# Kernel tuning notes

Hardware: AMD Instinct MI355X
Metric: run time of the kernel (lower is better)

The kernel has to match this reference:

```python
import jax, jax.numpy as jnp
import numpy as np

NUM_COLORS = 10
COLOR_MAPPING_W = 0.4
CONSISTENCY_W = 0.3
RULE_W = 0.2
EXACT_BONUS = 5.0


def _color_rules(targets, num_colors):
    # Vectorized equivalent of per-batch torch.unique(): sorted unique colors
    # of each grid written into the first slots of a [B, 10] rules tensor.
    B = targets.shape[0]
    colors = jnp.arange(num_colors)
    presence = jnp.any(targets[:, :, :, None] == colors, axis=(1, 2))  # [B, 10]
    pos = jnp.cumsum(presence.astype(jnp.int32), axis=1) - 1           # slot index per color
    cols = jnp.where(presence, pos, num_colors)                        # absent -> dump slot
    rules = jnp.zeros((B, num_colors + 1), dtype=jnp.float32)
    rules = rules.at[jnp.arange(B)[:, None], cols].set(
        colors.astype(jnp.float32) * presence.astype(jnp.float32))
    return rules[:, :num_colors]


def setup_inputs() -> dict:
    key = jax.random.key(0)
    k1, k2, k3, k4 = jax.random.split(key, 4)
    B, C, H, W = 4096, NUM_COLORS, 30, 30
    return {
        "color_output": jax.random.normal(k1, (B, C, H, W), dtype=jnp.float32),
        "targets": jax.random.randint(k2, (B, H, W), 0, C),
        "color_attention": jax.random.uniform(k3, (B, H, W, C), dtype=jnp.float32),
        "lstm_rules": jax.random.normal(k4, (B, C), dtype=jnp.float32),
    }


def reference(color_output, targets, color_attention, lstm_rules):
    B, C, H, W = color_output.shape
    # exact-match cross entropy (mean over B*H*W)
    logp = jax.nn.log_softmax(color_output, axis=1)               # [B,C,H,W]
    ce = -jnp.take_along_axis(logp, targets[:, None], axis=1).mean()
    pred_colors = jnp.argmax(color_output, axis=1)                # [B,H,W]
    eq = (pred_colors == targets).astype(jnp.float32)
    exact_count = eq.sum()
    # color mapping: MSE(attention, one_hot(targets))
    onehot = jax.nn.one_hot(targets, C, dtype=jnp.float32)        # [B,H,W,C]
    color_mapping = jnp.mean((color_attention - onehot) ** 2)
    # sliding 2x2 window consistency, fused: avg over windows of (1 - mean eq)
    s = eq[:, :-1, :-1] + eq[:, 1:, :-1] + eq[:, :-1, 1:] + eq[:, 1:, 1:]
    consistency = 1.0 - s.mean() / 4.0
    # rule learning: MSE against per-batch sorted-unique-color rules
    rule_target = _color_rules(targets, C)
    rule_loss = jnp.mean((lstm_rules - rule_target) ** 2)
    total = (ce + COLOR_MAPPING_W * color_mapping
             + CONSISTENCY_W * consistency + RULE_W * rule_loss)
    total = total - (exact_count / B) * EXACT_BONUS  # bonus is 0 when count is 0
    total = jnp.maximum(total, 0.001)
    return (total, ce, color_mapping, consistency, rule_loss, exact_count)
```

## Files before the change

kernel.cpp:

```cpp
#include <hip/hip_runtime.h>


namespace {
constexpr int kB = 4096;
constexpr int kC = 10;
constexpr int kH = 30;
constexpr int kW = 30;
constexpr int kHW = kH * kW;
constexpr int kCHW = kC * kHW;
constexpr int kThreads = 256;
constexpr int kP4 = kHW / 4;
}

__global__ __launch_bounds__(kThreads) void iris_main(
    const float* __restrict__ logits_g,
    const int* __restrict__ targets_g,
    const float* __restrict__ att_g,
    const float* __restrict__ rules_g,
    float* __restrict__ ce_part,
    float* __restrict__ cm_part,
    unsigned* __restrict__ weq_part,
    unsigned* __restrict__ eq_part,
    float* __restrict__ rule_part)
{
    const int b = blockIdx.x;
    const int tid = threadIdx.x;
    const float* __restrict__ logits = logits_g + (size_t)b * kCHW;
    const int* __restrict__ tgt = targets_g + (size_t)b * kHW;
    const float* __restrict__ att = att_g + (size_t)b * (kHW * kC);

    float ce_acc = 0.f, cm_acc = 0.f;
    unsigned weq_acc = 0u, eq_acc = 0u, mask_acc = 0u;

    if (tid < kP4) {
        const int p0 = tid * 4;

        const int4 tv = *reinterpret_cast<const int4*>(tgt + p0);
        const int ta[4] = {tv.x, tv.y, tv.z, tv.w};
        mask_acc = (1u << ta[0]) | (1u << ta[1]) | (1u << ta[2]) | (1u << ta[3]);

        float x[kC][4];
#pragma unroll
        for (int c = 0; c < kC; ++c) {
            const float4 v = *reinterpret_cast<const float4*>(logits + c * kHW + p0);
            x[c][0] = v.x; x[c][1] = v.y; x[c][2] = v.z; x[c][3] = v.w;
        }

        float xm[4], xt[4];
        int am[4];
#pragma unroll
        for (int j = 0; j < 4; ++j) { xm[j] = -3.4e38f; xt[j] = 0.f; am[j] = 0; }
#pragma unroll
        for (int c = 0; c < kC; ++c) {
#pragma unroll
            for (int j = 0; j < 4; ++j) {
                const bool gt = x[c][j] > xm[j];
                am[j] = gt ? c : am[j];
                xm[j] = gt ? x[c][j] : xm[j];
                xt[j] = (c == ta[j]) ? x[c][j] : xt[j];
            }
        }
#pragma unroll
        for (int j = 0; j < 4; ++j) {
            float s = 0.f;
#pragma unroll
            for (int c = 0; c < kC; ++c) s += __expf(x[c][j] - xm[j]);
            ce_acc += xm[j] + __logf(s) - xt[j];

            const unsigned eq = (am[j] == ta[j]) ? 1u : 0u;
            eq_acc += eq;
            const int p = p0 + j;
            const int h = p / kW;
            const int w = p - h * kW;
            const unsigned wgt = ((h == 0 || h == kH - 1) ? 1u : 2u) *
                                 ((w == 0 || w == kW - 1) ? 1u : 2u);
            weq_acc += eq * wgt;
        }

        const float* __restrict__ a = att + (size_t)p0 * kC;
        float at[4] = {0.f, 0.f, 0.f, 0.f};
        float sq = 0.f;
#pragma unroll
        for (int i = 0; i < kC; ++i) {
            const float4 v = *reinterpret_cast<const float4*>(a + i * 4);
            const float av[4] = {v.x, v.y, v.z, v.w};
#pragma unroll
            for (int k = 0; k < 4; ++k) {
                const int e = 4 * i + k;
                const int j = e / kC;
                const int ch = e - j * kC;
                sq += av[k] * av[k];
                at[j] = (ch == ta[j]) ? av[k] : at[j];
            }
        }
        cm_acc = sq - 2.f * (at[0] + at[1] + at[2] + at[3]) + 4.f;
    }

#pragma unroll
    for (int off = 32; off > 0; off >>= 1) {
        ce_acc  += __shfl_down(ce_acc, off);
        cm_acc  += __shfl_down(cm_acc, off);
        weq_acc += __shfl_down(weq_acc, off);
        eq_acc  += __shfl_down(eq_acc, off);
        mask_acc |= __shfl_down(mask_acc, off);
    }

    __shared__ float s_ce[4], s_cm[4];
    __shared__ unsigned s_weq[4], s_eq[4], s_mask[4];
    const int wave = tid >> 6;
    if ((tid & 63) == 0) {
        s_ce[wave] = ce_acc;
        s_cm[wave] = cm_acc;
        s_weq[wave] = weq_acc;
        s_eq[wave] = eq_acc;
        s_mask[wave] = mask_acc;
    }
    __syncthreads();

    if (tid == 0) {
        ce_part[b]  = s_ce[0] + s_ce[1] + s_ce[2] + s_ce[3];
        cm_part[b]  = s_cm[0] + s_cm[1] + s_cm[2] + s_cm[3];
        weq_part[b] = s_weq[0] + s_weq[1] + s_weq[2] + s_weq[3];
        eq_part[b]  = s_eq[0] + s_eq[1] + s_eq[2] + s_eq[3];
        const unsigned mask = s_mask[0] | s_mask[1] | s_mask[2] | s_mask[3];

        const float* __restrict__ lr = rules_g + (size_t)b * kC;
        unsigned mrem = mask;
        float rl = 0.f;
#pragma unroll
        for (int s2 = 0; s2 < kC; ++s2) {
            float v = 0.f;
            if (mrem) {
                v = (float)(__ffs(mrem) - 1);
                mrem &= mrem - 1u;
            }
            const float d = lr[s2] - v;
            rl += d * d;
        }
        rule_part[b] = rl;
    }
}

__global__ __launch_bounds__(256) void iris_finalize(
    const float* __restrict__ ce_part,
    const float* __restrict__ cm_part,
    const unsigned* __restrict__ weq_part,
    const unsigned* __restrict__ eq_part,
    const float* __restrict__ rule_part,
    float* __restrict__ out)
{
    const int tid = threadIdx.x;
    double ce = 0.0, cm = 0.0, rl = 0.0;
    unsigned long long weq = 0ull, eqc = 0ull;
    for (int i = tid; i < kB; i += 256) {
        ce += (double)ce_part[i];
        cm += (double)cm_part[i];
        rl += (double)rule_part[i];
        weq += (unsigned long long)weq_part[i];
        eqc += (unsigned long long)eq_part[i];
    }
#pragma unroll
    for (int off = 32; off > 0; off >>= 1) {
        ce  += __shfl_down(ce, off);
        cm  += __shfl_down(cm, off);
        rl  += __shfl_down(rl, off);
        weq += __shfl_down(weq, off);
        eqc += __shfl_down(eqc, off);
    }
    __shared__ double sd[3][4];
    __shared__ unsigned long long su[2][4];
    const int wave = tid >> 6;
    if ((tid & 63) == 0) {
        sd[0][wave] = ce; sd[1][wave] = cm; sd[2][wave] = rl;
        su[0][wave] = weq; su[1][wave] = eqc;
    }
    __syncthreads();
    if (tid == 0) {
        ce  = sd[0][0] + sd[0][1] + sd[0][2] + sd[0][3];
        cm  = sd[1][0] + sd[1][1] + sd[1][2] + sd[1][3];
        rl  = sd[2][0] + sd[2][1] + sd[2][2] + sd[2][3];
        weq = su[0][0] + su[0][1] + su[0][2] + su[0][3];
        eqc = su[1][0] + su[1][1] + su[1][2] + su[1][3];

        const double ce_m = ce / ((double)kB * kHW);
        const double cm_m = cm / ((double)kB * kHW * kC);
        const double s_mean = (double)weq / ((double)kB * (kH - 1) * (kW - 1));
        const double cons = 1.0 - s_mean / 4.0;
        const double rl_m = rl / ((double)kB * kC);
        const double exact = (double)eqc;
        double total = ce_m + 0.4 * cm_m + 0.3 * cons + 0.2 * rl_m
                       - (exact / (double)kB) * 5.0;
        if (total < 0.001) total = 0.001;
        out[0] = (float)total;
        out[1] = (float)ce_m;
        out[2] = (float)cm_m;
        out[3] = (float)cons;
        out[4] = (float)rl_m;
        out[5] = (float)exact;
    }
}

extern "C" void kernel_launch(void* const* d_in, const int* in_sizes, int n_in,
                              void* d_out, int out_size, void* d_ws, size_t ws_size,
                              hipStream_t stream) {
    const float* color_output    = (const float*)d_in[0];
    const int*   targets         = (const int*)d_in[1];
    const float* color_attention = (const float*)d_in[2];
    const float* lstm_rules      = (const float*)d_in[3];
    float* out = (float*)d_out;

    float*    ce_part   = (float*)d_ws;
    float*    cm_part   = ce_part + kB;
    unsigned* weq_part  = (unsigned*)(cm_part + kB);
    unsigned* eq_part   = weq_part + kB;
    float*    rule_part = (float*)(eq_part + kB);

    iris_main<<<kB, kThreads, 0, stream>>>(color_output, targets, color_attention,
                                           lstm_rules, ce_part, cm_part,
                                           weq_part, eq_part, rule_part);
    iris_finalize<<<1, 256, 0, stream>>>(ce_part, cm_part, weq_part, eq_part,
                                         rule_part, out);
}
```

Before: 325.6 us.

## Read attention with all threads coalesced and gather target values separately

The attention tensor is now streamed by all 256 threads with strided float4 loads, so the sum of squares covers the full block instead of only the 225 owner threads each reading 40 contiguous floats. The one-hot term becomes a per-pixel gather of the target channel, and the constant +1 per pixel moves into the finalize kernel. Occupancy hints are added via launch bounds, and finalize now uses 1024 threads with an unrolled loop. The cost is extra scattered gather loads for the target channel, and a sched_barrier that constrains instruction scheduling.

```diff
diff --git a/kernel.cpp b/kernel.cpp
--- a/kernel.cpp
+++ b/kernel.cpp
@@ -10,9 +10,10 @@
 constexpr int kCHW = kC * kHW;
 constexpr int kThreads = 256;
 constexpr int kP4 = kHW / 4;
-}
-
-__global__ __launch_bounds__(kThreads) void iris_main(
+constexpr int kF4 = kCHW / 4;
+}
+
+__global__ __launch_bounds__(kThreads, 4) void iris_main(
     const float* __restrict__ logits_g,
     const int* __restrict__ targets_g,
     const float* __restrict__ att_g,
@@ -27,24 +28,48 @@
     const int tid = threadIdx.x;
     const float* __restrict__ logits = logits_g + (size_t)b * kCHW;
     const int* __restrict__ tgt = targets_g + (size_t)b * kHW;
-    const float* __restrict__ att = att_g + (size_t)b * (kHW * kC);
+    const float* __restrict__ att = att_g + (size_t)b * kCHW;
 
     float ce_acc = 0.f, cm_acc = 0.f;
     unsigned weq_acc = 0u, eq_acc = 0u, mask_acc = 0u;
 
-    if (tid < kP4) {
-        const int p0 = tid * 4;
-
+    const bool owner = (tid < kP4);
+    const int p0 = tid * 4;
+
+    int ta[4] = {0, 0, 0, 0};
+    float x[kC][4];
+    float atg[4] = {0.f, 0.f, 0.f, 0.f};
+    if (owner) {
         const int4 tv = *reinterpret_cast<const int4*>(tgt + p0);
-        const int ta[4] = {tv.x, tv.y, tv.z, tv.w};
-        mask_acc = (1u << ta[0]) | (1u << ta[1]) | (1u << ta[2]) | (1u << ta[3]);
-
-        float x[kC][4];
+        ta[0] = tv.x; ta[1] = tv.y; ta[2] = tv.z; ta[3] = tv.w;
 #pragma unroll
         for (int c = 0; c < kC; ++c) {
             const float4 v = *reinterpret_cast<const float4*>(logits + c * kHW + p0);
             x[c][0] = v.x; x[c][1] = v.y; x[c][2] = v.z; x[c][3] = v.w;
         }
+        mask_acc = (1u << ta[0]) | (1u << ta[1]) | (1u << ta[2]) | (1u << ta[3]);
+#pragma unroll
+        for (int j = 0; j < 4; ++j)
+            atg[j] = att[(p0 + j) * kC + ta[j]];
+    }
+    __builtin_amdgcn_sched_barrier(0);
+
+    {
+        float sq = 0.f;
+#pragma unroll
+        for (int k = 0; k < 8; ++k) {
+            const float4 v = *reinterpret_cast<const float4*>(att + 4 * (tid + kThreads * k));
+            sq += v.x * v.x + v.y * v.y + v.z * v.z + v.w * v.w;
+        }
+        if (tid < kF4 - 8 * kThreads) {
+            const float4 v = *reinterpret_cast<const float4*>(att + 4 * (tid + kThreads * 8));
+            sq += v.x * v.x + v.y * v.y + v.z * v.z + v.w * v.w;
+        }
+        cm_acc = sq;
+    }
+
+    if (owner) {
+        cm_acc -= 2.f * (atg[0] + atg[1] + atg[2] + atg[3]);
 
         float xm[4], xt[4];
         int am[4];
@@ -76,24 +101,6 @@
                                  ((w == 0 || w == kW - 1) ? 1u : 2u);
             weq_acc += eq * wgt;
         }
-
-        const float* __restrict__ a = att + (size_t)p0 * kC;
-        float at[4] = {0.f, 0.f, 0.f, 0.f};
-        float sq = 0.f;
-#pragma unroll
-        for (int i = 0; i < kC; ++i) {
-            const float4 v = *reinterpret_cast<const float4*>(a + i * 4);
-            const float av[4] = {v.x, v.y, v.z, v.w};
-#pragma unroll
-            for (int k = 0; k < 4; ++k) {
-                const int e = 4 * i + k;
-                const int j = e / kC;
-                const int ch = e - j * kC;
-                sq += av[k] * av[k];
-                at[j] = (ch == ta[j]) ? av[k] : at[j];
-            }
-        }
-        cm_acc = sq - 2.f * (at[0] + at[1] + at[2] + at[3]) + 4.f;
     }
 
 #pragma unroll
@@ -141,7 +148,7 @@
     }
 }
 
-__global__ __launch_bounds__(256) void iris_finalize(
+__global__ __launch_bounds__(1024) void iris_finalize(
     const float* __restrict__ ce_part,
     const float* __restrict__ cm_part,
     const unsigned* __restrict__ weq_part,
@@ -152,7 +159,9 @@
     const int tid = threadIdx.x;
     double ce = 0.0, cm = 0.0, rl = 0.0;
     unsigned long long weq = 0ull, eqc = 0ull;
-    for (int i = tid; i < kB; i += 256) {
+#pragma unroll
+    for (int k = 0; k < 4; ++k) {
+        const int i = tid + 1024 * k;
         ce += (double)ce_part[i];
         cm += (double)cm_part[i];
         rl += (double)rule_part[i];
@@ -167,8 +176,8 @@
         weq += __shfl_down(weq, off);
         eqc += __shfl_down(eqc, off);
     }
-    __shared__ double sd[3][4];
-    __shared__ unsigned long long su[2][4];
+    __shared__ double sd[3][16];
+    __shared__ unsigned long long su[2][16];
     const int wave = tid >> 6;
     if ((tid & 63) == 0) {
         sd[0][wave] = ce; sd[1][wave] = cm; sd[2][wave] = rl;
@@ -176,14 +185,14 @@
     }
     __syncthreads();
     if (tid == 0) {
-        ce  = sd[0][0] + sd[0][1] + sd[0][2] + sd[0][3];
-        cm  = sd[1][0] + sd[1][1] + sd[1][2] + sd[1][3];
-        rl  = sd[2][0] + sd[2][1] + sd[2][2] + sd[2][3];
-        weq = su[0][0] + su[0][1] + su[0][2] + su[0][3];
-        eqc = su[1][0] + su[1][1] + su[1][2] + su[1][3];
-
+        ce = 0.0; cm = 0.0; rl = 0.0; weq = 0ull; eqc = 0ull;
+#pragma unroll
+        for (int i = 0; i < 16; ++i) {
+            ce += sd[0][i]; cm += sd[1][i]; rl += sd[2][i];
+            weq += su[0][i]; eqc += su[1][i];
+        }
         const double ce_m = ce / ((double)kB * kHW);
-        const double cm_m = cm / ((double)kB * kHW * kC);
+        const double cm_m = (cm + (double)kB * kHW) / ((double)kB * kHW * kC);
         const double s_mean = (double)weq / ((double)kB * (kH - 1) * (kW - 1));
         const double cons = 1.0 - s_mean / 4.0;
         const double rl_m = rl / ((double)kB * kC);
@@ -218,6 +227,6 @@
     iris_main<<<kB, kThreads, 0, stream>>>(color_output, targets, color_attention,
                                            lstm_rules, ce_part, cm_part,
                                            weq_part, eq_part, rule_part);
-    iris_finalize<<<1, 256, 0, stream>>>(ce_part, cm_part, weq_part, eq_part,
-                                         rule_part, out);
-}
+    iris_finalize<<<1, 1024, 0, stream>>>(ce_part, cm_part, weq_part, eq_part,
+                                          rule_part, out);
+}
```

Result: faster. 315.9 us (-3.0%).
